# Kernel optimization log

Hardware: AMD Instinct MI355X
Metric: run time of the kernel (lower is better)

The kernel has to match this reference:

```python
import jax, jax.numpy as jnp
import numpy as np

B, H, S, D = 2, 16, 2048, 64  # batch, heads, seq_len (= hist_len), head_dim
NEG = -1.0e9


def setup_inputs() -> dict:
    key = jax.random.key(0)
    kq, kk, kv = jax.random.split(key, 3)
    q = jax.random.normal(kq, (B, H, S, D), dtype=jnp.float32)
    k = jax.random.normal(kk, (B, H, S, D), dtype=jnp.float32)
    v = jax.random.normal(kv, (B, H, S, D), dtype=jnp.float32)
    return {"q": q, "k": k, "v": v}


def _ghostmax(scores):
    # softmax with an extra implicit zero logit: exp(s)/(1 + sum exp(s)), stable form
    m = jnp.maximum(jnp.max(scores, axis=-1, keepdims=True), 0.0)
    e = jnp.exp(scores - m)
    denom = jnp.sum(e, axis=-1, keepdims=True) + jnp.exp(-m)
    return e / denom


def reference(q, k, v):
    scaling = 1.0 / np.sqrt(D).astype(np.float32)
    # [B,H,S,S] score matrix (fully materialized, as in the torch module)
    scores = jnp.einsum('bhqd,bhkd->bhqk', q, k) * scaling
    # causal mask: additive -1e9 above the diagonal (block_ids is None)
    causal_mask = jnp.triu(jnp.full((S, S), NEG, dtype=scores.dtype), k=1)
    scores = scores + causal_mask  # broadcast over [B,H]
    weights = _ghostmax(scores)
    # dropout p=0.0 -> identity
    return jnp.einsum('bhqk,bhkd->bhqd', weights, v)
```

## Files before the change

### kernel.cpp

```cpp
#include <hip/hip_runtime.h>

typedef __attribute__((ext_vector_type(8))) short bf16x8;
typedef __attribute__((ext_vector_type(4))) float f32x4;
typedef __attribute__((ext_vector_type(16))) float f32x16;

union BFU { uint4 q; bf16x8 v; };

__device__ __forceinline__ unsigned short f2bf(float f) {
  unsigned u = __float_as_uint(f);
  u += 0x7fff + ((u >> 16) & 1);
  return (unsigned short)(u >> 16);
}
__device__ __forceinline__ unsigned pk2(float a, float b) {
  return (unsigned)f2bf(a) | ((unsigned)f2bf(b) << 16);
}
__device__ __forceinline__ unsigned cvtpk(float lo, float hi) {
  unsigned d;
  asm("v_cvt_pk_bf16_f32 %0, %1, %2" : "=v"(d) : "v"(lo), "v"(hi));
  return d;
}
__device__ __forceinline__ float xhalf_sum(float x) {
  return x + __shfl_xor(x, 32);
}
#if __has_builtin(__builtin_amdgcn_exp2f)
__device__ __forceinline__ float fexp2(float x) { return __builtin_amdgcn_exp2f(x); }
#else
__device__ __forceinline__ float fexp2(float x) {
  float r;
  asm("v_exp_f32 %0, %1\n\ts_nop 1" : "=v"(r) : "v"(x));
  return r;
}
#endif

#define S_LEN 2048
#define DH 64
#define LOG2E 1.4426950408889634f

__global__ __launch_bounds__(256) void prepack(const float* __restrict__ K,
                                               const float* __restrict__ V,
                                               unsigned char* __restrict__ wsK,
                                               unsigned char* __restrict__ wsVt) {
  const int t = threadIdx.x;
  const int bid = blockIdx.x;
  const size_t gbase = (size_t)bid * 4096;
  const int row = t & 63;
  const int j = t >> 6;
  unsigned char* obK = wsK + (size_t)bid * 8192;
  unsigned char* obV = wsVt + (size_t)bid * 8192;
#pragma unroll
  for (int gg = 0; gg < 2; ++gg) {
    const int g = j + gg * 4;
    {
      const float* kg = K + gbase + (size_t)row * DH + g * 8;
      float4 x = *(const float4*)kg;
      float4 y = *(const float4*)(kg + 4);
      uint4 h;
      h.x = pk2(x.x, x.y); h.y = pk2(x.z, x.w);
      h.z = pk2(y.x, y.y); h.w = pk2(y.z, y.w);
      *(uint4*)(obK + g * 1024 + row * 16) = h;
    }
    {
      const float* vg = V + gbase + row;
      float v0 = vg[(size_t)(g * 8 + 0) * DH], v1 = vg[(size_t)(g * 8 + 1) * DH];
      float v2 = vg[(size_t)(g * 8 + 2) * DH], v3 = vg[(size_t)(g * 8 + 3) * DH];
      float v4 = vg[(size_t)(g * 8 + 4) * DH], v5 = vg[(size_t)(g * 8 + 5) * DH];
      float v6 = vg[(size_t)(g * 8 + 6) * DH], v7 = vg[(size_t)(g * 8 + 7) * DH];
      uint4 h;
      h.x = pk2(v0, v1); h.y = pk2(v2, v3);
      h.z = pk2(v4, v5); h.w = pk2(v6, v7);
      *(uint4*)(obV + g * 1024 + row * 16) = h;
    }
  }
}

__global__ __launch_bounds__(128) void fattn17(const float* __restrict__ Q,
                                               const unsigned char* __restrict__ wsK,
                                               const unsigned char* __restrict__ wsVt,
                                               float* __restrict__ O) {
  __shared__ float mlds[64][34];
  const int t = threadIdx.x;
  const int lane = t & 63;
  const int w = t >> 6;
  const int c = lane & 31;
  const int hi = lane >> 5;

  const int bid = blockIdx.x;
  const int bh = bid & 31;
  const int qt = 63 - (bid >> 5);

  const float* qrow = Q + ((size_t)(bh * S_LEN) + qt * 32 + c) * DH;
  BFU qf[4];
#pragma unroll
  for (int i = 0; i < 4; ++i) {
    const int d0 = i * 16 + hi * 8;
    float4 x = *(const float4*)(qrow + d0);
    float4 y = *(const float4*)(qrow + d0 + 4);
    const float sc = 0.125f * LOG2E;
    qf[i].q.x = pk2(x.x * sc, x.y * sc);
    qf[i].q.y = pk2(x.z * sc, x.w * sc);
    qf[i].q.z = pk2(y.x * sc, y.y * sc);
    qf[i].q.w = pk2(y.z * sc, y.w * sc);
  }

  f32x16 acc0, acc1;
#pragma unroll
  for (int r = 0; r < 16; ++r) { acc0[r] = 0.f; acc1[r] = 0.f; }
  float sacc[4] = {0.f, 0.f, 0.f, 0.f};

  const unsigned char* tbK = wsK + (size_t)bh * 32 * 8192;
  const unsigned char* tbV = wsVt + (size_t)bh * 32 * 8192;
  const int fo = hi * 1024 + c * 16;

  const int NT = (qt + 1) >> 1;
  const int last = qt >> 1;
  const int NTH = NT - (NT >> 1);
  const int t0 = w ? NTH : 0;
  const int t1 = w ? NT : NTH;
  const int lastL = w ? last : (NTH - 1);
  const bool dotail = (!(qt & 1)) && (w == 1);

  BFU kf0[4], kf1[4], vf0[4], vf1[4];
#define LOADK(tile_)                                                       \
  {                                                                        \
    const unsigned char* kb_ = tbK + (size_t)(tile_) * 8192;               \
    _Pragma("unroll")                                                      \
    for (int i = 0; i < 4; ++i) {                                          \
      kf0[i].q = *(const uint4*)(kb_ + i * 2048 + fo);                     \
      kf1[i].q = *(const uint4*)(kb_ + i * 2048 + fo + 512);               \
    }                                                                      \
  }
#define LOADV(tile_)                                                       \
  {                                                                        \
    const unsigned char* vb_ = tbV + (size_t)(tile_) * 8192;               \
    _Pragma("unroll")                                                      \
    for (int i = 0; i < 4; ++i) {                                          \
      vf0[i].q = *(const uint4*)(vb_ + i * 2048 + fo);                     \
      vf1[i].q = *(const uint4*)(vb_ + i * 2048 + fo + 512);               \
    }                                                                      \
  }
#define MAKEPF(dst, x0, x1, x2, x3, y0, y1, y2, y3)                  \
    {                                                                \
      unsigned a01 = cvtpk(x0, x1), a23 = cvtpk(x2, x3);             \
      unsigned b01 = cvtpk(y0, y1), b23 = cvtpk(y2, y3);             \
      asm("v_permlane32_swap_b32 %0, %1" : "+v"(a01), "+v"(b01));    \
      asm("v_permlane32_swap_b32 %0, %1" : "+v"(a23), "+v"(b23));    \
      (dst).q.x = a01; (dst).q.y = a23; (dst).q.z = b01; (dst).q.w = b23; \
    }

  LOADK(t0)
  LOADV(t0)

  for (int kt = t0; kt < t1; ++kt) {
    f32x16 st0, st1;
#pragma unroll
    for (int r = 0; r < 16; ++r) { st0[r] = 0.f; st1[r] = 0.f; }
    __builtin_amdgcn_s_setprio(1);
#pragma unroll
    for (int i = 0; i < 4; ++i) {
      st0 = __builtin_amdgcn_mfma_f32_32x32x16_bf16(kf0[i].v, qf[i].v, st0, 0, 0, 0);
      st1 = __builtin_amdgcn_mfma_f32_32x32x16_bf16(kf1[i].v, qf[i].v, st1, 0, 0, 0);
    }
    __builtin_amdgcn_s_setprio(0);

    if (kt + 1 <= lastL) LOADK(kt + 1)

    if ((qt & 1) && kt == NT - 1) {
#pragma unroll
      for (int r = 0; r < 16; ++r) {
        const int kvloc = (r & 3) + 8 * (r >> 2) + 4 * hi;
        if (kvloc > c) st1[r] = -1e9f;
      }
    }

#pragma unroll
    for (int r = 0; r < 16; ++r) { st0[r] = fexp2(st0[r]); st1[r] = fexp2(st1[r]); }
#pragma unroll
    for (int r = 0; r < 16; ++r) sacc[r & 3] += st0[r] + st1[r];

    BFU pf[4];
    MAKEPF(pf[0], st0[0], st0[1], st0[2], st0[3], st0[4], st0[5], st0[6], st0[7])
    MAKEPF(pf[1], st0[8], st0[9], st0[10], st0[11], st0[12], st0[13], st0[14], st0[15])
    MAKEPF(pf[2], st1[0], st1[1], st1[2], st1[3], st1[4], st1[5], st1[6], st1[7])
    MAKEPF(pf[3], st1[8], st1[9], st1[10], st1[11], st1[12], st1[13], st1[14], st1[15])

    __builtin_amdgcn_s_setprio(1);
#pragma unroll
    for (int kvt = 0; kvt < 4; ++kvt) {
      acc0 = __builtin_amdgcn_mfma_f32_32x32x16_bf16(vf0[kvt].v, pf[kvt].v, acc0, 0, 0, 0);
      acc1 = __builtin_amdgcn_mfma_f32_32x32x16_bf16(vf1[kvt].v, pf[kvt].v, acc1, 0, 0, 0);
    }
    __builtin_amdgcn_s_setprio(0);

    if (kt + 1 <= lastL) LOADV(kt + 1)
  }

  if (dotail) {
    f32x16 st0;
#pragma unroll
    for (int r = 0; r < 16; ++r) st0[r] = 0.f;
    __builtin_amdgcn_s_setprio(1);
#pragma unroll
    for (int i = 0; i < 4; ++i)
      st0 = __builtin_amdgcn_mfma_f32_32x32x16_bf16(kf0[i].v, qf[i].v, st0, 0, 0, 0);
    __builtin_amdgcn_s_setprio(0);
#pragma unroll
    for (int r = 0; r < 16; ++r) {
      const int kvloc = (r & 3) + 8 * (r >> 2) + 4 * hi;
      st0[r] = (kvloc > c) ? 0.f : fexp2(st0[r]);
    }
#pragma unroll
    for (int r = 0; r < 16; ++r) sacc[r & 3] += st0[r];
    BFU pf0, pf1;
    MAKEPF(pf0, st0[0], st0[1], st0[2], st0[3], st0[4], st0[5], st0[6], st0[7])
    MAKEPF(pf1, st0[8], st0[9], st0[10], st0[11], st0[12], st0[13], st0[14], st0[15])
    __builtin_amdgcn_s_setprio(1);
    acc0 = __builtin_amdgcn_mfma_f32_32x32x16_bf16(vf0[0].v, pf0.v, acc0, 0, 0, 0);
    acc0 = __builtin_amdgcn_mfma_f32_32x32x16_bf16(vf0[1].v, pf1.v, acc0, 0, 0, 0);
    acc1 = __builtin_amdgcn_mfma_f32_32x32x16_bf16(vf1[0].v, pf0.v, acc1, 0, 0, 0);
    acc1 = __builtin_amdgcn_mfma_f32_32x32x16_bf16(vf1[1].v, pf1.v, acc1, 0, 0, 0);
    __builtin_amdgcn_s_setprio(0);
  }
#undef MAKEPF
#undef LOADK
#undef LOADV

  const float lpart = (sacc[0] + sacc[1]) + (sacc[2] + sacc[3]);

  if (w == 1) {
#pragma unroll
    for (int r = 0; r < 16; ++r) { mlds[lane][r] = acc0[r]; mlds[lane][16 + r] = acc1[r]; }
    mlds[lane][32] = lpart;
  }
  __syncthreads();
  if (w == 0) {
#pragma unroll
    for (int r = 0; r < 16; ++r) { acc0[r] += mlds[lane][r]; acc1[r] += mlds[lane][16 + r]; }
    const float lrun = 1.f + xhalf_sum(lpart + mlds[lane][32]);
    const float inv = 1.f / lrun;
    float* orow = O + ((size_t)(bh * S_LEN) + qt * 32 + c) * DH;
#pragma unroll
    for (int k = 0; k < 4; ++k) {
      float4 o0, o1;
      o0.x = acc0[4 * k] * inv;     o0.y = acc0[4 * k + 1] * inv;
      o0.z = acc0[4 * k + 2] * inv; o0.w = acc0[4 * k + 3] * inv;
      o1.x = acc1[4 * k] * inv;     o1.y = acc1[4 * k + 1] * inv;
      o1.z = acc1[4 * k + 2] * inv; o1.w = acc1[4 * k + 3] * inv;
      *(float4*)(orow + 8 * k + 4 * hi) = o0;
      *(float4*)(orow + 32 + 8 * k + 4 * hi) = o1;
    }
  }
}

__global__ __launch_bounds__(256) void fattn_fb(const float* __restrict__ Q,
                                                const float* __restrict__ K,
                                                const float* __restrict__ V,
                                                float* __restrict__ O) {
  __shared__ __align__(16) unsigned char lds[24 * 1024];
  unsigned char* kb = lds;
  unsigned char* vb = lds + 8192;
  const int t = threadIdx.x;
  const int lane = t & 63;
  const int w = t >> 6;
  const int g = lane >> 4;
  const int n = lane & 15;
  unsigned char* pb = lds + 16384 + w * 2048;

  const int bid = blockIdx.x;
  const int bh = bid & 31;
  const int qt = bid >> 5;
  const int q0 = qt * 64;

  const float* qg = Q + ((size_t)(bh * S_LEN) + q0 + w * 16 + n) * DH + g * 8;
  BFU qf[2];
#pragma unroll
  for (int cc = 0; cc < 2; ++cc) {
    float4 x = *(const float4*)(qg + 32 * cc);
    float4 y = *(const float4*)(qg + 32 * cc + 4);
    const float sc = 0.125f * LOG2E;
    qf[cc].q.x = pk2(x.x * sc, x.y * sc);
    qf[cc].q.y = pk2(x.z * sc, x.w * sc);
    qf[cc].q.z = pk2(y.x * sc, y.y * sc);
    qf[cc].q.w = pk2(y.z * sc, y.w * sc);
  }

  f32x4 acc[4] = {{0.f,0.f,0.f,0.f},{0.f,0.f,0.f,0.f},{0.f,0.f,0.f,0.f},{0.f,0.f,0.f,0.f}};
  float mrun[4] = {0.f, 0.f, 0.f, 0.f};
  float lrun[4] = {1.f, 1.f, 1.f, 1.f};

  const int sr = t >> 2;
  const int dc = (t & 3) * 16;
  const size_t kvbase = (size_t)(bh * S_LEN) * DH;

  for (int kt = 0; kt <= qt; ++kt) {
    __syncthreads();
    {
      const float* kg = K + kvbase + (size_t)(kt * 64 + sr) * DH + dc;
      float4 k0 = *(const float4*)(kg);
      float4 k1 = *(const float4*)(kg + 4);
      float4 k2 = *(const float4*)(kg + 8);
      float4 k3 = *(const float4*)(kg + 12);
      uint4 h0, h1;
      h0.x = pk2(k0.x, k0.y); h0.y = pk2(k0.z, k0.w);
      h0.z = pk2(k1.x, k1.y); h0.w = pk2(k1.z, k1.w);
      h1.x = pk2(k2.x, k2.y); h1.y = pk2(k2.z, k2.w);
      h1.z = pk2(k3.x, k3.y); h1.w = pk2(k3.z, k3.w);
      const int kbase = sr * 128 + dc * 2;
      const int ksw = (sr & 7) << 4;
      *(uint4*)(kb + ((kbase) ^ ksw)) = h0;
      *(uint4*)(kb + ((kbase + 16) ^ ksw)) = h1;

      const float* vg = V + kvbase + (size_t)(kt * 64 + sr) * DH + dc;
      float4 v0 = *(const float4*)(vg);
      float4 v1 = *(const float4*)(vg + 4);
      float4 v2 = *(const float4*)(vg + 8);
      float4 v3 = *(const float4*)(vg + 12);
      const int r2 = sr * 2;
#define VW(j, val) { const int d_ = dc + (j); \
  *(unsigned short*)(vb + ((d_ * 128 + r2) ^ ((d_ & 7) << 4))) = f2bf(val); }
      VW(0, v0.x) VW(1, v0.y) VW(2, v0.z) VW(3, v0.w)
      VW(4, v1.x) VW(5, v1.y) VW(6, v1.z) VW(7, v1.w)
      VW(8, v2.x) VW(9, v2.y) VW(10, v2.z) VW(11, v2.w)
      VW(12, v3.x) VW(13, v3.y) VW(14, v3.z) VW(15, v3.w)
#undef VW
    }
    __syncthreads();

    f32x4 sv[4] = {{0.f,0.f,0.f,0.f},{0.f,0.f,0.f,0.f},{0.f,0.f,0.f,0.f},{0.f,0.f,0.f,0.f}};
#pragma unroll
    for (int cc = 0; cc < 2; ++cc) {
#pragma unroll
      for (int nt = 0; nt < 4; ++nt) {
        const int kv = nt * 16 + n;
        BFU kf;
        kf.q = *(const uint4*)(kb + ((kv * 128 + g * 16 + cc * 64) ^ ((kv & 7) << 4)));
        sv[nt] = __builtin_amdgcn_mfma_f32_16x16x32_bf16(qf[cc].v, kf.v, sv[nt], 0, 0, 0);
      }
    }

    if (kt == qt) {
#pragma unroll
      for (int nt = 0; nt < 4; ++nt)
#pragma unroll
        for (int r = 0; r < 4; ++r)
          if (nt * 16 + n > w * 16 + g * 4 + r) sv[nt][r] = -1e9f;
    }

#pragma unroll
    for (int r = 0; r < 4; ++r) {
      float s0 = sv[0][r], s1 = sv[1][r], s2 = sv[2][r], s3 = sv[3][r];
      float mx = fmaxf(fmaxf(s0, s1), fmaxf(s2, s3));
#pragma unroll
      for (int off = 1; off < 16; off <<= 1) mx = fmaxf(mx, __shfl_xor(mx, off));
      const float mnew = fmaxf(mrun[r], mx);
      const float p0 = fexp2(s0 - mnew);
      const float p1 = fexp2(s1 - mnew);
      const float p2 = fexp2(s2 - mnew);
      const float p3 = fexp2(s3 - mnew);
      float sum = (p0 + p1) + (p2 + p3);
#pragma unroll
      for (int off = 1; off < 16; off <<= 1) sum += __shfl_xor(sum, off);
      const float scale = fexp2(mrun[r] - mnew);
      lrun[r] = lrun[r] * scale + sum;
      mrun[r] = mnew;
      acc[0][r] *= scale; acc[1][r] *= scale; acc[2][r] *= scale; acc[3][r] *= scale;
      const int row = g * 4 + r;
      const int rb = row * 128;
      const int sw = (row & 7) << 4;
      *(unsigned short*)(pb + ((rb + (0 * 16 + n) * 2) ^ sw)) = f2bf(p0);
      *(unsigned short*)(pb + ((rb + (1 * 16 + n) * 2) ^ sw)) = f2bf(p1);
      *(unsigned short*)(pb + ((rb + (2 * 16 + n) * 2) ^ sw)) = f2bf(p2);
      *(unsigned short*)(pb + ((rb + (3 * 16 + n) * 2) ^ sw)) = f2bf(p3);
    }

#pragma unroll
    for (int cc = 0; cc < 2; ++cc) {
      BFU pfr;
      pfr.q = *(const uint4*)(pb + ((n * 128 + g * 16 + cc * 64) ^ ((n & 7) << 4)));
#pragma unroll
      for (int nt = 0; nt < 4; ++nt) {
        const int d_ = nt * 16 + n;
        BFU vf;
        vf.q = *(const uint4*)(vb + ((d_ * 128 + g * 16 + cc * 64) ^ ((d_ & 7) << 4)));
        acc[nt] = __builtin_amdgcn_mfma_f32_16x16x32_bf16(pfr.v, vf.v, acc[nt], 0, 0, 0);
      }
    }
  }

#pragma unroll
  for (int r = 0; r < 4; ++r) {
    const float inv = 1.f / lrun[r];
    float* op = O + ((size_t)(bh * S_LEN) + q0 + w * 16 + g * 4 + r) * DH + n;
    op[0]  = acc[0][r] * inv;
    op[16] = acc[1][r] * inv;
    op[32] = acc[2][r] * inv;
    op[48] = acc[3][r] * inv;
  }
}

extern "C" void kernel_launch(void* const* d_in, const int* in_sizes, int n_in,
                              void* d_out, int out_size, void* d_ws, size_t ws_size,
                              hipStream_t stream) {
  const float* Q = (const float*)d_in[0];
  const float* K = (const float*)d_in[1];
  const float* V = (const float*)d_in[2];
  float* O = (float*)d_out;
  const size_t need_pack = (size_t)1024 * 8192 * 2;
  if (ws_size >= need_pack) {
    unsigned char* wsK = (unsigned char*)d_ws;
    unsigned char* wsVt = wsK + (size_t)1024 * 8192;
    prepack<<<dim3(1024), dim3(256), 0, stream>>>(K, V, wsK, wsVt);
    fattn17<<<dim3(2048), dim3(128), 0, stream>>>(Q, wsK, wsVt, O);
  } else {
    fattn_fb<<<dim3(1024), dim3(256), 0, stream>>>(Q, K, V, O);
  }
}
```

Baseline: 47.24 us.

## Share double-buffered LDS K/V tiles between two query-tile waves per block

Each 2-wave block now processes two adjacent 32-row query tiles, one per wave, instead of splitting one query tile's KV range across the waves. K/V tiles are staged into double-buffered LDS with global_load_lds, so both waves reuse one global fetch. This halves the grid and removes the cross-wave LDS reduction of accumulators. In exchange it adds a __syncthreads per KV tile, LDS reads, and less parallelism per query tile, which may hurt latency hiding for long causal rows.

```diff
diff --git a/kernel.cpp b/kernel.cpp
--- a/kernel.cpp
+++ b/kernel.cpp
@@ -31,6 +31,11 @@
   return r;
 }
 #endif
+__device__ __forceinline__ void gld16(const void* g, void* l) {
+  __builtin_amdgcn_global_load_lds(
+      (const __attribute__((address_space(1))) unsigned int*)g,
+      (__attribute__((address_space(3))) unsigned int*)l, 16, 0, 0);
+}
 
 #define S_LEN 2048
 #define DH 64
@@ -73,11 +78,11 @@
   }
 }
 
-__global__ __launch_bounds__(128) void fattn17(const float* __restrict__ Q,
+__global__ __launch_bounds__(128) void fattn18(const float* __restrict__ Q,
                                                const unsigned char* __restrict__ wsK,
                                                const unsigned char* __restrict__ wsVt,
                                                float* __restrict__ O) {
-  __shared__ float mlds[64][34];
+  __shared__ __align__(16) unsigned char lds[2 * 16384];
   const int t = threadIdx.x;
   const int lane = t & 63;
   const int w = t >> 6;
@@ -86,7 +91,8 @@
 
   const int bid = blockIdx.x;
   const int bh = bid & 31;
-  const int qt = 63 - (bid >> 5);
+  const int u = 31 - (bid >> 5);
+  const int qt = 2 * u + w;
 
   const float* qrow = Q + ((size_t)(bh * S_LEN) + qt * 32 + c) * DH;
   BFU qf[4];
@@ -105,38 +111,43 @@
   f32x16 acc0, acc1;
 #pragma unroll
   for (int r = 0; r < 16; ++r) { acc0[r] = 0.f; acc1[r] = 0.f; }
-  float sacc[4] = {0.f, 0.f, 0.f, 0.f};
+  float sacc[16];
+#pragma unroll
+  for (int r = 0; r < 16; ++r) sacc[r] = 0.f;
 
   const unsigned char* tbK = wsK + (size_t)bh * 32 * 8192;
   const unsigned char* tbV = wsVt + (size_t)bh * 32 * 8192;
   const int fo = hi * 1024 + c * 16;
-
-  const int NT = (qt + 1) >> 1;
-  const int last = qt >> 1;
-  const int NTH = NT - (NT >> 1);
-  const int t0 = w ? NTH : 0;
-  const int t1 = w ? NT : NTH;
-  const int lastL = w ? last : (NTH - 1);
-  const bool dotail = (!(qt & 1)) && (w == 1);
-
-  BFU kf0[4], kf1[4], vf0[4], vf1[4];
-#define LOADK(tile_)                                                       \
-  {                                                                        \
-    const unsigned char* kb_ = tbK + (size_t)(tile_) * 8192;               \
-    _Pragma("unroll")                                                      \
-    for (int i = 0; i < 4; ++i) {                                          \
-      kf0[i].q = *(const uint4*)(kb_ + i * 2048 + fo);                     \
-      kf1[i].q = *(const uint4*)(kb_ + i * 2048 + fo + 512);               \
-    }                                                                      \
-  }
-#define LOADV(tile_)                                                       \
-  {                                                                        \
-    const unsigned char* vb_ = tbV + (size_t)(tile_) * 8192;               \
-    _Pragma("unroll")                                                      \
-    for (int i = 0; i < 4; ++i) {                                          \
-      vf0[i].q = *(const uint4*)(vb_ + i * 2048 + fo);                     \
-      vf1[i].q = *(const uint4*)(vb_ + i * 2048 + fo + 512);               \
-    }                                                                      \
+  const int so = t * 16;
+
+#define STAGE(buf_, kt_)                                                    \
+  {                                                                         \
+    const unsigned char* sK = tbK + (size_t)(kt_) * 8192;                   \
+    const unsigned char* sV = tbV + (size_t)(kt_) * 8192;                   \
+    unsigned char* dK = lds + (buf_) * 16384;                               \
+    unsigned char* dV = dK + 8192;                                          \
+    _Pragma("unroll")                                                       \
+    for (int j = 0; j < 4; ++j) gld16(sK + j * 2048 + so, dK + j * 2048 + so); \
+    _Pragma("unroll")                                                       \
+    for (int j = 0; j < 4; ++j) gld16(sV + j * 2048 + so, dV + j * 2048 + so); \
+  }
+#define LDSK(buf_)                                                          \
+  {                                                                         \
+    const unsigned char* kb_ = lds + (buf_) * 16384;                        \
+    _Pragma("unroll")                                                       \
+    for (int i = 0; i < 4; ++i) {                                           \
+      kf0[i].q = *(const uint4*)(kb_ + i * 2048 + fo);                      \
+      kf1[i].q = *(const uint4*)(kb_ + i * 2048 + fo + 512);                \
+    }                                                                       \
+  }
+#define LDSV(buf_)                                                          \
+  {                                                                         \
+    const unsigned char* vb_ = lds + (buf_) * 16384 + 8192;                 \
+    _Pragma("unroll")                                                       \
+    for (int i = 0; i < 4; ++i) {                                           \
+      vf0[i].q = *(const uint4*)(vb_ + i * 2048 + fo);                      \
+      vf1[i].q = *(const uint4*)(vb_ + i * 2048 + fo + 512);                \
+    }                                                                       \
   }
 #define MAKEPF(dst, x0, x1, x2, x3, y0, y1, y2, y3)                  \
     {                                                                \
@@ -147,107 +158,110 @@
       (dst).q.x = a01; (dst).q.y = a23; (dst).q.z = b01; (dst).q.w = b23; \
     }
 
-  LOADK(t0)
-  LOADV(t0)
-
-  for (int kt = t0; kt < t1; ++kt) {
-    f32x16 st0, st1;
-#pragma unroll
-    for (int r = 0; r < 16; ++r) { st0[r] = 0.f; st1[r] = 0.f; }
-    __builtin_amdgcn_s_setprio(1);
-#pragma unroll
-    for (int i = 0; i < 4; ++i) {
-      st0 = __builtin_amdgcn_mfma_f32_32x32x16_bf16(kf0[i].v, qf[i].v, st0, 0, 0, 0);
-      st1 = __builtin_amdgcn_mfma_f32_32x32x16_bf16(kf1[i].v, qf[i].v, st1, 0, 0, 0);
-    }
-    __builtin_amdgcn_s_setprio(0);
-
-    if (kt + 1 <= lastL) LOADK(kt + 1)
-
-    if ((qt & 1) && kt == NT - 1) {
+  BFU kf0[4], kf1[4], vf0[4], vf1[4];
+
+  STAGE(0, 0)
+  __syncthreads();
+
+  int cur = 0;
+  for (int kt = 0; kt <= u; ++kt) {
+    if (kt < u) STAGE(cur ^ 1, kt + 1)
+
+    LDSK(cur)
+    LDSV(cur)
+
+    const bool a_tail = (w == 0) && (kt == u);
+    if (!a_tail) {
+      f32x16 st0, st1;
+#pragma unroll
+      for (int r = 0; r < 16; ++r) { st0[r] = 0.f; st1[r] = 0.f; }
+      __builtin_amdgcn_s_setprio(1);
+#pragma unroll
+      for (int i = 0; i < 4; ++i) {
+        st0 = __builtin_amdgcn_mfma_f32_32x32x16_bf16(kf0[i].v, qf[i].v, st0, 0, 0, 0);
+        st1 = __builtin_amdgcn_mfma_f32_32x32x16_bf16(kf1[i].v, qf[i].v, st1, 0, 0, 0);
+      }
+      __builtin_amdgcn_s_setprio(0);
+
+      if (w == 1 && kt == u) {
+#pragma unroll
+        for (int r = 0; r < 16; ++r) {
+          const int kvloc = (r & 3) + 8 * (r >> 2) + 4 * hi;
+          if (kvloc > c) st1[r] = -1e9f;
+        }
+      }
+
+#pragma unroll
+      for (int r = 0; r < 16; ++r) { st0[r] = fexp2(st0[r]); st1[r] = fexp2(st1[r]); }
+#pragma unroll
+      for (int r = 0; r < 16; ++r) sacc[r] += st0[r] + st1[r];
+
+      BFU pf[4];
+      MAKEPF(pf[0], st0[0], st0[1], st0[2], st0[3], st0[4], st0[5], st0[6], st0[7])
+      MAKEPF(pf[1], st0[8], st0[9], st0[10], st0[11], st0[12], st0[13], st0[14], st0[15])
+      MAKEPF(pf[2], st1[0], st1[1], st1[2], st1[3], st1[4], st1[5], st1[6], st1[7])
+      MAKEPF(pf[3], st1[8], st1[9], st1[10], st1[11], st1[12], st1[13], st1[14], st1[15])
+
+      __builtin_amdgcn_s_setprio(1);
+#pragma unroll
+      for (int kvt = 0; kvt < 4; ++kvt) {
+        acc0 = __builtin_amdgcn_mfma_f32_32x32x16_bf16(vf0[kvt].v, pf[kvt].v, acc0, 0, 0, 0);
+        acc1 = __builtin_amdgcn_mfma_f32_32x32x16_bf16(vf1[kvt].v, pf[kvt].v, acc1, 0, 0, 0);
+      }
+      __builtin_amdgcn_s_setprio(0);
+    } else {
+      f32x16 st0;
+#pragma unroll
+      for (int r = 0; r < 16; ++r) st0[r] = 0.f;
+      __builtin_amdgcn_s_setprio(1);
+#pragma unroll
+      for (int i = 0; i < 4; ++i)
+        st0 = __builtin_amdgcn_mfma_f32_32x32x16_bf16(kf0[i].v, qf[i].v, st0, 0, 0, 0);
+      __builtin_amdgcn_s_setprio(0);
 #pragma unroll
       for (int r = 0; r < 16; ++r) {
         const int kvloc = (r & 3) + 8 * (r >> 2) + 4 * hi;
-        if (kvloc > c) st1[r] = -1e9f;
-      }
-    }
-
-#pragma unroll
-    for (int r = 0; r < 16; ++r) { st0[r] = fexp2(st0[r]); st1[r] = fexp2(st1[r]); }
-#pragma unroll
-    for (int r = 0; r < 16; ++r) sacc[r & 3] += st0[r] + st1[r];
-
-    BFU pf[4];
-    MAKEPF(pf[0], st0[0], st0[1], st0[2], st0[3], st0[4], st0[5], st0[6], st0[7])
-    MAKEPF(pf[1], st0[8], st0[9], st0[10], st0[11], st0[12], st0[13], st0[14], st0[15])
-    MAKEPF(pf[2], st1[0], st1[1], st1[2], st1[3], st1[4], st1[5], st1[6], st1[7])
-    MAKEPF(pf[3], st1[8], st1[9], st1[10], st1[11], st1[12], st1[13], st1[14], st1[15])
-
-    __builtin_amdgcn_s_setprio(1);
-#pragma unroll
-    for (int kvt = 0; kvt < 4; ++kvt) {
-      acc0 = __builtin_amdgcn_mfma_f32_32x32x16_bf16(vf0[kvt].v, pf[kvt].v, acc0, 0, 0, 0);
-      acc1 = __builtin_amdgcn_mfma_f32_32x32x16_bf16(vf1[kvt].v, pf[kvt].v, acc1, 0, 0, 0);
-    }
-    __builtin_amdgcn_s_setprio(0);
-
-    if (kt + 1 <= lastL) LOADV(kt + 1)
-  }
-
-  if (dotail) {
-    f32x16 st0;
-#pragma unroll
-    for (int r = 0; r < 16; ++r) st0[r] = 0.f;
-    __builtin_amdgcn_s_setprio(1);
-#pragma unroll
-    for (int i = 0; i < 4; ++i)
-      st0 = __builtin_amdgcn_mfma_f32_32x32x16_bf16(kf0[i].v, qf[i].v, st0, 0, 0, 0);
-    __builtin_amdgcn_s_setprio(0);
-#pragma unroll
-    for (int r = 0; r < 16; ++r) {
-      const int kvloc = (r & 3) + 8 * (r >> 2) + 4 * hi;
-      st0[r] = (kvloc > c) ? 0.f : fexp2(st0[r]);
-    }
-#pragma unroll
-    for (int r = 0; r < 16; ++r) sacc[r & 3] += st0[r];
-    BFU pf0, pf1;
-    MAKEPF(pf0, st0[0], st0[1], st0[2], st0[3], st0[4], st0[5], st0[6], st0[7])
-    MAKEPF(pf1, st0[8], st0[9], st0[10], st0[11], st0[12], st0[13], st0[14], st0[15])
-    __builtin_amdgcn_s_setprio(1);
-    acc0 = __builtin_amdgcn_mfma_f32_32x32x16_bf16(vf0[0].v, pf0.v, acc0, 0, 0, 0);
-    acc0 = __builtin_amdgcn_mfma_f32_32x32x16_bf16(vf0[1].v, pf1.v, acc0, 0, 0, 0);
-    acc1 = __builtin_amdgcn_mfma_f32_32x32x16_bf16(vf1[0].v, pf0.v, acc1, 0, 0, 0);
-    acc1 = __builtin_amdgcn_mfma_f32_32x32x16_bf16(vf1[1].v, pf1.v, acc1, 0, 0, 0);
-    __builtin_amdgcn_s_setprio(0);
+        st0[r] = (kvloc > c) ? 0.f : fexp2(st0[r]);
+      }
+#pragma unroll
+      for (int r = 0; r < 16; ++r) sacc[r] += st0[r];
+      BFU pf0, pf1;
+      MAKEPF(pf0, st0[0], st0[1], st0[2], st0[3], st0[4], st0[5], st0[6], st0[7])
+      MAKEPF(pf1, st0[8], st0[9], st0[10], st0[11], st0[12], st0[13], st0[14], st0[15])
+      __builtin_amdgcn_s_setprio(1);
+      acc0 = __builtin_amdgcn_mfma_f32_32x32x16_bf16(vf0[0].v, pf0.v, acc0, 0, 0, 0);
+      acc0 = __builtin_amdgcn_mfma_f32_32x32x16_bf16(vf0[1].v, pf1.v, acc0, 0, 0, 0);
+      acc1 = __builtin_amdgcn_mfma_f32_32x32x16_bf16(vf1[0].v, pf0.v, acc1, 0, 0, 0);
+      acc1 = __builtin_amdgcn_mfma_f32_32x32x16_bf16(vf1[1].v, pf1.v, acc1, 0, 0, 0);
+      __builtin_amdgcn_s_setprio(0);
+    }
+
+    __syncthreads();
+    cur ^= 1;
   }
 #undef MAKEPF
-#undef LOADK
-#undef LOADV
-
-  const float lpart = (sacc[0] + sacc[1]) + (sacc[2] + sacc[3]);
-
-  if (w == 1) {
-#pragma unroll
-    for (int r = 0; r < 16; ++r) { mlds[lane][r] = acc0[r]; mlds[lane][16 + r] = acc1[r]; }
-    mlds[lane][32] = lpart;
-  }
-  __syncthreads();
-  if (w == 0) {
-#pragma unroll
-    for (int r = 0; r < 16; ++r) { acc0[r] += mlds[lane][r]; acc1[r] += mlds[lane][16 + r]; }
-    const float lrun = 1.f + xhalf_sum(lpart + mlds[lane][32]);
-    const float inv = 1.f / lrun;
-    float* orow = O + ((size_t)(bh * S_LEN) + qt * 32 + c) * DH;
-#pragma unroll
-    for (int k = 0; k < 4; ++k) {
-      float4 o0, o1;
-      o0.x = acc0[4 * k] * inv;     o0.y = acc0[4 * k + 1] * inv;
-      o0.z = acc0[4 * k + 2] * inv; o0.w = acc0[4 * k + 3] * inv;
-      o1.x = acc1[4 * k] * inv;     o1.y = acc1[4 * k + 1] * inv;
-      o1.z = acc1[4 * k + 2] * inv; o1.w = acc1[4 * k + 3] * inv;
-      *(float4*)(orow + 8 * k + 4 * hi) = o0;
-      *(float4*)(orow + 32 + 8 * k + 4 * hi) = o1;
-    }
+#undef LDSV
+#undef LDSK
+#undef STAGE
+
+#pragma unroll
+  for (int off = 8; off >= 1; off >>= 1)
+#pragma unroll
+    for (int r = 0; r < 8; ++r)
+      if (r < off) sacc[r] += sacc[r + off];
+  const float lrun = 1.f + xhalf_sum(sacc[0]);
+
+  const float inv = 1.f / lrun;
+  float* orow = O + ((size_t)(bh * S_LEN) + qt * 32 + c) * DH;
+#pragma unroll
+  for (int k = 0; k < 4; ++k) {
+    float4 o0, o1;
+    o0.x = acc0[4 * k] * inv;     o0.y = acc0[4 * k + 1] * inv;
+    o0.z = acc0[4 * k + 2] * inv; o0.w = acc0[4 * k + 3] * inv;
+    o1.x = acc1[4 * k] * inv;     o1.y = acc1[4 * k + 1] * inv;
+    o1.z = acc1[4 * k + 2] * inv; o1.w = acc1[4 * k + 3] * inv;
+    *(float4*)(orow + 8 * k + 4 * hi) = o0;
+    *(float4*)(orow + 32 + 8 * k + 4 * hi) = o1;
   }
 }
 
@@ -409,7 +423,7 @@
     unsigned char* wsK = (unsigned char*)d_ws;
     unsigned char* wsVt = wsK + (size_t)1024 * 8192;
     prepack<<<dim3(1024), dim3(256), 0, stream>>>(K, V, wsK, wsVt);
-    fattn17<<<dim3(2048), dim3(128), 0, stream>>>(Q, wsK, wsVt, O);
+    fattn18<<<dim3(1024), dim3(128), 0, stream>>>(Q, wsK, wsVt, O);
   } else {
     fattn_fb<<<dim3(1024), dim3(256), 0, stream>>>(Q, K, V, O);
   }
```

Result: slower. 55.17 us (+16.8%).
